# Optimization experiments

Measured on AMD Instinct MI355X. Metric: run time of the kernel, lower is better.

## Reference

```python
import jax, jax.numpy as jnp
import numpy as np

SEQ_LEN, N_VARS, N_SKILLS, D_IN = 120, 9, 32, 1
BATCH = 32768


def setup_inputs() -> dict:
    key = jax.random.key(0)
    ks = jax.random.split(key, 8)
    H, D = N_SKILLS, D_IN
    s = 1.0 / np.sqrt(H)  # torch LSTMCell init scale
    return {
        "x": jax.random.normal(ks[0], (BATCH, N_VARS * SEQ_LEN), dtype=jnp.float32),
        # nn.LSTMCell params (gate order i,f,g,o)
        "W_ih": jax.random.uniform(ks[1], (4 * H, D), jnp.float32, -s, s),
        "W_hh": jax.random.uniform(ks[2], (4 * H, H), jnp.float32, -s, s),
        "b_ih": jax.random.uniform(ks[3], (4 * H,), jnp.float32, -s, s),
        "b_hh": jax.random.uniform(ks[4], (4 * H,), jnp.float32, -s, s),
        # contextual gate params: cg_w Linear(D,H,bias=False), cg_u Linear(H,H)
        "cg_w": jax.random.uniform(ks[5], (H, D), jnp.float32, -s, s),
        "cg_u": jax.random.uniform(ks[6], (H, H), jnp.float32, -s, s),
        "cg_b": jax.random.uniform(ks[7], (H,), jnp.float32, -s, s),
    }


def reference(x, W_ih, W_hh, b_ih, b_hh, cg_w, cg_u, cg_b):
    B = x.shape[0]
    H = N_SKILLS
    # [B, V*T] -> fold the 9 independent variable-sequences into the batch dim
    # (the same cell weights are shared across vars), then scan over time.
    xs = x.reshape(B * N_VARS, SEQ_LEN, D_IN)
    xs = jnp.moveaxis(xs, 1, 0)  # [T, B*V, D_IN]

    def step(carry, xt):
        h, c = carry  # each [B*V, H]
        gates = xt @ W_ih.T + b_ih + h @ W_hh.T + b_hh  # [B*V, 4H]
        i, f, g, o = jnp.split(gates, 4, axis=-1)
        i = jax.nn.sigmoid(i)
        f = jax.nn.sigmoid(f)
        g = jnp.tanh(g)
        c_new = f * c + i * g
        # contextual gate uses the *previous* h
        cg = jax.nn.sigmoid(xt @ cg_w.T + h @ cg_u.T + cg_b)
        h_new = cg * jnp.tanh(c_new)
        return (h_new, c_new), None

    zeros = jnp.zeros((B * N_VARS, H), dtype=x.dtype)
    (h, _), _ = jax.lax.scan(step, (zeros, zeros), xs)
    # [B*V, H] -> [B, V*H] (variable-major, matching torch.cat over vars)
    return h.reshape(B, N_VARS * H)
```

## Files before the change

kernel.cpp:

```cpp
#include <hip/hip_runtime.h>


#define NV 9
#define TLEN 120
#define HS 32
#define BATCH_ 32768
#define NSEQ (BATCH_ * NV)
#define NBATCH (NSEQ / 16)
#define GRID_ 6144

#define XSTRIDE 20
#define HSTRIDE 36

#define LOG2E 1.4426950408889634f
#define TWOL  2.8853900817779268f

typedef __attribute__((ext_vector_type(8))) short bf16x8;
typedef __attribute__((ext_vector_type(4))) float f32x4;
typedef __attribute__((ext_vector_type(4))) unsigned int u32x4;

__device__ __forceinline__ float fast_exp2(float x) { return __builtin_amdgcn_exp2f(x); }
__device__ __forceinline__ float fast_rcp(float x)  { return __builtin_amdgcn_rcpf(x); }
__device__ __forceinline__ unsigned int fbits(float x) { return __builtin_bit_cast(unsigned int, x); }
__device__ __forceinline__ float bcastf(unsigned int x) { return __builtin_bit_cast(float, x); }

__device__ __forceinline__ f32x4 splat4(float x) { f32x4 v = {x, x, x, x}; return v; }
__device__ __forceinline__ f32x4 fma4(f32x4 a, f32x4 b, f32x4 c) {
  return __builtin_elementwise_fma(a, b, c);
}
__device__ __forceinline__ f32x4 exp24(f32x4 v) {
  f32x4 r;
  r[0] = fast_exp2(v[0]); r[1] = fast_exp2(v[1]);
  r[2] = fast_exp2(v[2]); r[3] = fast_exp2(v[3]);
  return r;
}
__device__ __forceinline__ f32x4 rcp4(f32x4 v) {
  f32x4 r;
  r[0] = fast_rcp(v[0]); r[1] = fast_rcp(v[1]);
  r[2] = fast_rcp(v[2]); r[3] = fast_rcp(v[3]);
  return r;
}

__device__ __forceinline__ void lstm_elem(f32x4 ai, f32x4 af, f32x4 ag, f32x4 ac,
                                          f32x4& ct, f32x4& h) {
  const f32x4 one4 = splat4(1.0f);
  f32x4 Ei = exp24(ai), Ef = exp24(af), Eg = exp24(ag), Ea = exp24(ac);
  f32x4 pi_ = Ei + one4, pf_ = Ef + one4, pg_ = Eg + one4, pa_ = Ea + one4;
  f32x4 u   = fma4(Eg, splat4(TWOL), splat4(-TWOL));
  f32x4 P   = pi_ * pg_;
  f32x4 tt  = pf_ * u;
  f32x4 num = fma4(ct, P, tt);
  f32x4 den = pf_ * P;
  ct = num * rcp4(den);
  f32x4 Ec  = exp24(ct);
  h = (one4 - Ec) * rcp4(pa_ * (Ec + one4));
}

__global__ __launch_bounds__(64, 2) void cglstm_kernel(
    const float* __restrict__ x,
    const float* __restrict__ W_ih,
    const float* __restrict__ W_hh,
    const float* __restrict__ b_ih,
    const float* __restrict__ b_hh,
    const float* __restrict__ cg_w,
    const float* __restrict__ cg_u,
    const float* __restrict__ cg_b,
    float* __restrict__ out)
{
  const int lane = threadIdx.x;
  const int col  = lane & 15;
  const int quad = lane >> 4;

  __shared__ __align__(16) float xT[TLEN * XSTRIDE];
  __shared__ unsigned int hbuf[16 * HSTRIDE];

  bf16x8 bhi[8], blo[8];
  float wx[8], bb[8];
#pragma unroll
  for (int tile = 0; tile < 8; ++tile) {
    const int n = col + (tile & 1) * 16;
    const float sc_ = ((tile >> 1) == 2) ? -TWOL : -LOG2E;
    const float* wrow = (tile < 6) ? (W_hh + (size_t)((tile >> 1) * HS + n) * HS)
                                   : (cg_u + (size_t)n * HS);
    bf16x8 vh, vl;
#pragma unroll
    for (int e = 0; e < 8; ++e) {
      float wv = wrow[quad * 8 + e] * sc_;
      unsigned int wbits = fbits(wv);
      float lo_f = wv - bcastf(wbits & 0xffff0000u);
      vh[e] = (short)(wbits >> 16);
      vl[e] = (short)(fbits(lo_f) >> 16);
    }
    bhi[tile] = vh; blo[tile] = vl;
    if (tile < 6) {
      const int gg = tile >> 1;
      wx[tile] = W_ih[gg * HS + n] * sc_;
      bb[tile] = (b_ih[gg * HS + n] + b_hh[gg * HS + n]) * sc_;
    } else {
      wx[tile] = cg_w[n] * sc_;
      bb[tile] = cg_b[n] * sc_;
    }
  }

  for (int p = blockIdx.x; p < NBATCH; p += GRID_) {
    const float4* xb = (const float4*)(x + (size_t)p * 16 * TLEN);
    for (int i = lane; i < 480; i += 64) {
      float4 v = xb[i];
      int f0 = i * 4;
      int s  = f0 / TLEN;
      int t0 = f0 - s * TLEN;
      xT[(t0 + 0) * XSTRIDE + s] = v.x;
      xT[(t0 + 1) * XSTRIDE + s] = v.y;
      xT[(t0 + 2) * XSTRIDE + s] = v.z;
      xT[(t0 + 3) * XSTRIDE + s] = v.w;
    }
    for (int i = lane; i < 16 * HSTRIDE; i += 64) hbuf[i] = 0u;
    f32x4 ct0 = splat4(0.f), ct1 = splat4(0.f), h0 = splat4(0.f), h1 = splat4(0.f);
    __syncthreads();

#pragma unroll 1
    for (int t = 0; t < TLEN; ++t) {
      f32x4 xt4 = *(const f32x4*)&xT[t * XSTRIDE + quad * 4];
      f32x4 acc[8];
#pragma unroll
      for (int tile = 0; tile < 8; ++tile)
        acc[tile] = fma4(splat4(wx[tile]), xt4, splat4(bb[tile]));
      const unsigned int* hrow = &hbuf[col * HSTRIDE + quad * 8];
      u32x4 wa = *(const u32x4*)hrow;
      u32x4 wz = *(const u32x4*)(hrow + 4);
      u32x4 hi4, lo4;
      hi4[0] = __builtin_amdgcn_perm(wa[1], wa[0], 0x05040100u);
      hi4[1] = __builtin_amdgcn_perm(wa[3], wa[2], 0x05040100u);
      hi4[2] = __builtin_amdgcn_perm(wz[1], wz[0], 0x05040100u);
      hi4[3] = __builtin_amdgcn_perm(wz[3], wz[2], 0x05040100u);
      lo4[0] = __builtin_amdgcn_perm(wa[1], wa[0], 0x07060302u);
      lo4[1] = __builtin_amdgcn_perm(wa[3], wa[2], 0x07060302u);
      lo4[2] = __builtin_amdgcn_perm(wz[1], wz[0], 0x07060302u);
      lo4[3] = __builtin_amdgcn_perm(wz[3], wz[2], 0x07060302u);
      bf16x8 ahi = __builtin_bit_cast(bf16x8, hi4);
      bf16x8 alo = __builtin_bit_cast(bf16x8, lo4);
#pragma unroll
      for (int tile = 0; tile < 8; ++tile) {
        acc[tile] = __builtin_amdgcn_mfma_f32_16x16x32_bf16(ahi, bhi[tile], acc[tile], 0, 0, 0);
        acc[tile] = __builtin_amdgcn_mfma_f32_16x16x32_bf16(alo, bhi[tile], acc[tile], 0, 0, 0);
        acc[tile] = __builtin_amdgcn_mfma_f32_16x16x32_bf16(ahi, blo[tile], acc[tile], 0, 0, 0);
      }
      lstm_elem(acc[0], acc[2], acc[4], acc[6], ct0, h0);
      lstm_elem(acc[1], acc[3], acc[5], acc[7], ct1, h1);
#pragma unroll
      for (int r = 0; r < 4; ++r) {
        unsigned int hbits = fbits(h0[r]);
        float lof = h0[r] - bcastf(hbits & 0xffff0000u);
        hbuf[(quad * 4 + r) * HSTRIDE + col] =
            __builtin_amdgcn_perm(fbits(lof), hbits, 0x07060302u);
        unsigned int hbits1 = fbits(h1[r]);
        float lof1 = h1[r] - bcastf(hbits1 & 0xffff0000u);
        hbuf[(quad * 4 + r) * HSTRIDE + col + 16] =
            __builtin_amdgcn_perm(fbits(lof1), hbits1, 0x07060302u);
      }
      __syncthreads();
    }

    float* ob = out + (size_t)p * 16 * HS;
#pragma unroll
    for (int r = 0; r < 4; ++r) {
      ob[(quad * 4 + r) * HS + col]      = h0[r];
      ob[(quad * 4 + r) * HS + col + 16] = h1[r];
    }
    __syncthreads();
  }
}

extern "C" void kernel_launch(void* const* d_in, const int* in_sizes, int n_in,
                              void* d_out, int out_size, void* d_ws, size_t ws_size,
                              hipStream_t stream) {
  const float* x    = (const float*)d_in[0];
  const float* W_ih = (const float*)d_in[1];
  const float* W_hh = (const float*)d_in[2];
  const float* b_ih = (const float*)d_in[3];
  const float* b_hh = (const float*)d_in[4];
  const float* cg_w = (const float*)d_in[5];
  const float* cg_u = (const float*)d_in[6];
  const float* cg_b = (const float*)d_in[7];
  float* out = (float*)d_out;

  dim3 grid(GRID_), block(64);
  hipLaunchKernelGGL(cglstm_kernel, grid, block, 0, stream,
                     x, W_ih, W_hh, b_ih, b_hh, cg_w, cg_u, cg_b, out);
}
```

Baseline: 1.394 ms.

## Pack four independent waves per block and drop per-step block barriers

Each 256-thread block now holds four waves. Each wave owns one 16-sequence batch with its own private LDS slices for x and h. Because every wave only exchanges h with itself, the per-timestep __syncthreads is removed, and the grid-stride loop becomes a single batch per wave. The x staging is split into two 60-step chunks to shrink LDS per wave, which lets more waves share a CU. The code relies on in-order LDS access within a wave for correctness, with no explicit wave barrier.

```diff
diff --git a/kernel.cpp b/kernel.cpp
--- a/kernel.cpp
+++ b/kernel.cpp
@@ -7,8 +7,10 @@
 #define BATCH_ 32768
 #define NSEQ (BATCH_ * NV)
 #define NBATCH (NSEQ / 16)
-#define GRID_ 6144
+#define WPB 4
+#define GRID_ (NBATCH / WPB)
 
+#define TCHUNK 60
 #define XSTRIDE 20
 #define HSTRIDE 36
 
@@ -56,7 +58,7 @@
   h = (one4 - Ec) * rcp4(pa_ * (Ec + one4));
 }
 
-__global__ __launch_bounds__(64, 2) void cglstm_kernel(
+__global__ __launch_bounds__(256, 4) void cglstm_kernel(
     const float* __restrict__ x,
     const float* __restrict__ W_ih,
     const float* __restrict__ W_hh,
@@ -67,12 +69,15 @@
     const float* __restrict__ cg_b,
     float* __restrict__ out)
 {
-  const int lane = threadIdx.x;
+  const int lane = threadIdx.x & 63;
+  const int wid  = threadIdx.x >> 6;
   const int col  = lane & 15;
   const int quad = lane >> 4;
 
-  __shared__ __align__(16) float xT[TLEN * XSTRIDE];
-  __shared__ unsigned int hbuf[16 * HSTRIDE];
+  __shared__ __align__(16) float xT[WPB][TCHUNK * XSTRIDE];
+  __shared__ unsigned int hbuf[WPB][16 * HSTRIDE];
+  float* __restrict__ xTw = xT[wid];
+  unsigned int* hb = hbuf[wid];
 
   bf16x8 bhi[8], blo[8];
   float wx[8], bb[8];
@@ -102,30 +107,33 @@
     }
   }
 
-  for (int p = blockIdx.x; p < NBATCH; p += GRID_) {
-    const float4* xb = (const float4*)(x + (size_t)p * 16 * TLEN);
-    for (int i = lane; i < 480; i += 64) {
-      float4 v = xb[i];
-      int f0 = i * 4;
-      int s  = f0 / TLEN;
-      int t0 = f0 - s * TLEN;
-      xT[(t0 + 0) * XSTRIDE + s] = v.x;
-      xT[(t0 + 1) * XSTRIDE + s] = v.y;
-      xT[(t0 + 2) * XSTRIDE + s] = v.z;
-      xT[(t0 + 3) * XSTRIDE + s] = v.w;
-    }
-    for (int i = lane; i < 16 * HSTRIDE; i += 64) hbuf[i] = 0u;
-    f32x4 ct0 = splat4(0.f), ct1 = splat4(0.f), h0 = splat4(0.f), h1 = splat4(0.f);
-    __syncthreads();
+  const int p = blockIdx.x * WPB + wid;
+  const float4* xb = (const float4*)(x + (size_t)p * 16 * TLEN);
+
+  for (int i = lane; i < 16 * HSTRIDE; i += 64) hb[i] = 0u;
+  f32x4 ct0 = splat4(0.f), ct1 = splat4(0.f), h0 = splat4(0.f), h1 = splat4(0.f);
 
 #pragma unroll 1
-    for (int t = 0; t < TLEN; ++t) {
-      f32x4 xt4 = *(const f32x4*)&xT[t * XSTRIDE + quad * 4];
+  for (int chunk = 0; chunk < 2; ++chunk) {
+    for (int i = lane; i < 240; i += 64) {
+      int s = i / 15;
+      int j = i - s * 15;
+      float4 v = xb[s * 30 + chunk * 15 + j];
+      int t0 = j * 4;
+      xTw[(t0 + 0) * XSTRIDE + s] = v.x;
+      xTw[(t0 + 1) * XSTRIDE + s] = v.y;
+      xTw[(t0 + 2) * XSTRIDE + s] = v.z;
+      xTw[(t0 + 3) * XSTRIDE + s] = v.w;
+    }
+
+#pragma unroll 1
+    for (int tl = 0; tl < TCHUNK; ++tl) {
+      f32x4 xt4 = *(const f32x4*)&xTw[tl * XSTRIDE + quad * 4];
       f32x4 acc[8];
 #pragma unroll
       for (int tile = 0; tile < 8; ++tile)
         acc[tile] = fma4(splat4(wx[tile]), xt4, splat4(bb[tile]));
-      const unsigned int* hrow = &hbuf[col * HSTRIDE + quad * 8];
+      const unsigned int* hrow = &hb[col * HSTRIDE + quad * 8];
       u32x4 wa = *(const u32x4*)hrow;
       u32x4 wz = *(const u32x4*)(hrow + 4);
       u32x4 hi4, lo4;
@@ -151,23 +159,21 @@
       for (int r = 0; r < 4; ++r) {
         unsigned int hbits = fbits(h0[r]);
         float lof = h0[r] - bcastf(hbits & 0xffff0000u);
-        hbuf[(quad * 4 + r) * HSTRIDE + col] =
+        hb[(quad * 4 + r) * HSTRIDE + col] =
             __builtin_amdgcn_perm(fbits(lof), hbits, 0x07060302u);
         unsigned int hbits1 = fbits(h1[r]);
         float lof1 = h1[r] - bcastf(hbits1 & 0xffff0000u);
-        hbuf[(quad * 4 + r) * HSTRIDE + col + 16] =
+        hb[(quad * 4 + r) * HSTRIDE + col + 16] =
             __builtin_amdgcn_perm(fbits(lof1), hbits1, 0x07060302u);
       }
-      __syncthreads();
     }
+  }
 
-    float* ob = out + (size_t)p * 16 * HS;
+  float* ob = out + (size_t)p * 16 * HS;
 #pragma unroll
-    for (int r = 0; r < 4; ++r) {
-      ob[(quad * 4 + r) * HS + col]      = h0[r];
-      ob[(quad * 4 + r) * HS + col + 16] = h1[r];
-    }
-    __syncthreads();
+  for (int r = 0; r < 4; ++r) {
+    ob[(quad * 4 + r) * HS + col]      = h0[r];
+    ob[(quad * 4 + r) * HS + col + 16] = h1[r];
   }
 }
 
@@ -184,7 +190,7 @@
   const float* cg_b = (const float*)d_in[7];
   float* out = (float*)d_out;
 
-  dim3 grid(GRID_), block(64);
+  dim3 grid(GRID_), block(256);
   hipLaunchKernelGGL(cglstm_kernel, grid, block, 0, stream,
                      x, W_ih, W_hh, b_ih, b_hh, cg_w, cg_u, cg_b, out);
 }
```

After: 4.884 ms. +250.3%, slower.
